# Kernel optimization log

Measured on AMD Instinct MI355X. Metric: run time of the kernel, lower is better.

## Reference

```python
import jax, jax.numpy as jnp
import numpy as np

N, B, D, K, H = 30000, 16, 32, 8, 8
DIST = 5.0
EPS = 1e-6


def setup_inputs() -> dict:
    key = jax.random.key(0)
    ks = jax.random.split(key, 16)
    sc = 1.0 / np.sqrt(D)
    inp = {
        'pos': jax.random.uniform(ks[0], (N, 3), jnp.float32) * 20.0,
        'node_features': jax.random.normal(ks[1], (N, D), jnp.float32),
        'batch': jnp.sort(jax.random.randint(ks[2], (N,), 0, B, dtype=jnp.int32)),
        'bessel_weights': jnp.linspace(jnp.pi, K * jnp.pi, K).astype(jnp.float32),
        'init_dummy': jax.random.normal(ks[3], (D,), jnp.float32),
        'Wq_dummy': jax.random.normal(ks[4], (D, D), jnp.float32) * sc,
        'Wq_graph': jax.random.normal(ks[5], (D, D), jnp.float32) * sc,
        'Wdot': jax.random.normal(ks[6], (D, D), jnp.float32) * sc,
        'W1_kd': jax.random.normal(ks[7], (K, H), jnp.float32) / np.sqrt(K),
        'W2_kd': jax.random.normal(ks[8], (H, D * D), jnp.float32) / np.sqrt(H),
        'W1_vd': jax.random.normal(ks[9], (K, H), jnp.float32) / np.sqrt(K),
        'W2_vd': jax.random.normal(ks[10], (H, D * D), jnp.float32) / np.sqrt(H),
        'W1_kg': jax.random.normal(ks[11], (K, H), jnp.float32) / np.sqrt(K),
        'W2_kg': jax.random.normal(ks[12], (H, D * D), jnp.float32) / np.sqrt(H),
        'W1_vg': jax.random.normal(ks[13], (K, H), jnp.float32) / np.sqrt(K),
        'W2_vg': jax.random.normal(ks[14], (H, D * D), jnp.float32) / np.sqrt(H),
    }
    return inp


def reference(pos, node_features, batch, bessel_weights, init_dummy,
              Wq_dummy, Wq_graph, Wdot,
              W1_kd, W2_kd, W1_vd, W2_vd, W1_kg, W2_kg, W1_vg, W2_vg):
    scale = 1.0 / np.sqrt(D)

    # --- dummy edge features: per-batch z extents + bessel basis ---
    z = pos[:, 2]                                            # [N]
    z_min = jax.ops.segment_min(z, batch, num_segments=B)    # [B]
    z_max = jax.ops.segment_max(z, batch, num_segments=B)    # [B]
    bot_len = z - z_min[batch] + DIST                        # [N]
    top_len = z_max[batch] + DIST - z                        # [N]

    def bessel(x):  # [N] -> [N,K]
        return jnp.sin(bessel_weights * x[:, None]) / (x[:, None] + EPS)

    edge = jnp.stack([bessel(bot_len), bessel(top_len)], axis=1)  # [N,2,K]

    # --- init dummy node features [B, 2, D] ---
    dummy = jnp.broadcast_to(init_dummy, (B, 2, D))

    def gen_w(W1, W2):  # conditional weight generator (silu MLP)
        return (jax.nn.silu(edge @ W1) @ W2).reshape(N, 2, D, D)

    # --- dummy nodes attend over graph nodes (segment softmax) ---
    wk = gen_w(W1_kd, W2_kd)                                 # [N,2,D,D]
    wv = gen_w(W1_vd, W2_vd)
    q = (dummy @ Wq_dummy)[batch]                            # [N,2,D]
    k = jnp.einsum('nd,nsde->nse', node_features, wk)        # [N,2,D]
    v = jnp.einsum('nd,nsde->nse', node_features, wv)
    s = jnp.einsum('nsq,qk,nsk->ns', q, Wdot, k) * scale     # [N,2]
    m = jax.ops.segment_max(s, batch, num_segments=B)
    e = jnp.exp(s - m[batch])
    zsum = jax.ops.segment_sum(e, batch, num_segments=B)
    attn = e / zsum[batch]                                   # [N,2]
    dummy_new = dummy + jax.ops.segment_sum(attn[..., None] * v, batch, num_segments=B)

    # --- graph nodes attend over (2) dummy nodes ---
    wkg = gen_w(W1_kg, W2_kg)
    wvg = gen_w(W1_vg, W2_vg)
    d_per = dummy_new[batch]                                 # [N,2,D]
    kg = jnp.einsum('nsd,nsde->nse', d_per, wkg)
    vg = jnp.einsum('nsd,nsde->nse', d_per, wvg)
    qg = node_features @ Wq_graph                            # [N,D]
    sg = jnp.einsum('nq,qk,nsk->ns', qg, Wdot, kg) * scale   # [N,2]
    ag = jax.nn.softmax(sg, axis=1)
    x_new = node_features + jnp.einsum('ns,nsd->nd', ag, vg)  # [N,D]
    return x_new
```

## Files before the change

### kernel.cpp

```cpp
#include <hip/hip_runtime.h>
#include <math.h>

#define NN 30000
#define BB 16
#define DD 32
#define KK 8
#define HH 8
#define DIST_C 5.0f
#define EPS_C 1e-6f
#define SCALE_C 0.17677669529663687f

#define WS_ZMIN 0
#define WS_ZMAX 16
#define WS_ZSUM 32
#define WS_QW   64
#define WS_PK   96
#define WS_WC   352
#define WS_T    1376
#define WS_AKG  9568
#define WS_AVG  17760

#define NPB 32

__device__ __forceinline__ unsigned fencode(float f) {
    unsigned u = __float_as_uint(f);
    return (u & 0x80000000u) ? ~u : (u | 0x80000000u);
}
__device__ __forceinline__ float fdecode(unsigned c) {
    return __uint_as_float((c & 0x80000000u) ? (c ^ 0x80000000u) : ~c);
}
__device__ __forceinline__ float silu(float x) { return x / (1.0f + expf(-x)); }

__device__ __forceinline__ void bessel_edges(float bw0, float x0, float x1, float edge[2][8]) {
    float xs[2]; xs[0] = x0; xs[1] = x1;
    #pragma unroll
    for (int s = 0; s < 2; ++s) {
        float x = xs[s];
        float inv = 1.0f / (x + EPS_C);
        float th = bw0 * x;
        float c2 = 2.0f * cosf(th);
        float skm1 = 0.0f;
        float sk = sinf(th);
        #pragma unroll
        for (int k = 0; k < 8; ++k) {
            edge[s][k] = sk * inv;
            float nx = c2 * sk - skm1;
            skm1 = sk;
            sk = nx;
        }
    }
}

__global__ __launch_bounds__(256) void k_init(const float* __restrict__ init_dummy,
                                              const float* __restrict__ Wq_dummy,
                                              const float* __restrict__ Wdot,
                                              const float* __restrict__ W2_kd,
                                              const float* __restrict__ Wq_graph,
                                              float* __restrict__ ws) {
    __shared__ float qvec[32];
    __shared__ float qWl[32];
    int t = threadIdx.x;
    unsigned* wsu = (unsigned*)ws;
    if (t < 16) { wsu[WS_ZMIN + t] = 0xFFFFFFFFu; wsu[WS_ZMAX + t] = 0u; }
    if (t < 32) ws[WS_ZSUM + t] = 0.0f;
    for (int i = t; i < 8192; i += 256) ws[WS_T + i] = 0.0f;
    if (t < 32) {
        float acc = 0.0f;
        for (int d = 0; d < 32; ++d) acc += init_dummy[d] * Wq_dummy[d * 32 + t];
        qvec[t] = acc;
    }
    __syncthreads();
    if (t < 32) {
        float acc = 0.0f;
        for (int e = 0; e < 32; ++e) acc += qvec[e] * Wdot[e * 32 + t];
        qWl[t] = acc;
        ws[WS_QW + t] = acc;
    }
    __syncthreads();
    {
        int h = t >> 5, d = t & 31;
        float acc = 0.0f;
        for (int e = 0; e < 32; ++e) acc += W2_kd[h * 1024 + d * 32 + e] * qWl[e];
        ws[WS_PK + t] = acc;
    }
    for (int i = t; i < 1024; i += 256) {
        int d = i >> 5, e = i & 31;
        float acc = 0.0f;
        for (int m = 0; m < 32; ++m) acc += Wq_graph[d * 32 + m] * Wdot[m * 32 + e];
        ws[WS_WC + i] = acc;
    }
}

__global__ __launch_bounds__(256) void k_zminmax(const float* __restrict__ pos,
                                                 const int* __restrict__ batch,
                                                 float* __restrict__ ws) {
    __shared__ unsigned zl[16], zh[16];
    int t = threadIdx.x;
    if (t < 16) { zl[t] = 0xFFFFFFFFu; zh[t] = 0u; }
    __syncthreads();
    int n = blockIdx.x * 256 + t;
    if (n < NN) {
        unsigned c = fencode(pos[3 * n + 2]);
        int b = batch[n];
        atomicMin(&zl[b], c);
        atomicMax(&zh[b], c);
    }
    __syncthreads();
    unsigned* wsu = (unsigned*)ws;
    if (t < 16) {
        if (zl[t] != 0xFFFFFFFFu) atomicMin(&wsu[WS_ZMIN + t], zl[t]);
        if (zh[t] != 0u)          atomicMax(&wsu[WS_ZMAX + t], zh[t]);
    }
}

__global__ __launch_bounds__(256) void k_phase1(const float* __restrict__ pos,
                                                const int* __restrict__ batch,
                                                const float* __restrict__ nf,
                                                const float* __restrict__ bw,
                                                const float* __restrict__ W1_kd,
                                                const float* __restrict__ W1_vd,
                                                float* __restrict__ ws) {
    __shared__ __align__(16) float Fl[NPB * 36];
    __shared__ float Lw[NPB * 17];
    __shared__ int   Lb[NPB];
    __shared__ __align__(16) float Pk[256];
    __shared__ float W1kd[64], W1vd[64], zsl[32];
    int t = threadIdx.x;
    if (t < 64) { W1kd[t] = W1_kd[t]; W1vd[t] = W1_vd[t]; }
    Pk[t] = ws[WS_PK + t];
    if (t < 32) zsl[t] = 0.0f;

    int li = t >> 3, g = t & 7;
    int n0 = blockIdx.x * NPB;
    int n = n0 + li;
    bool valid = n < NN;
    float4 fv4 = make_float4(0.f, 0.f, 0.f, 0.f);
    int b = 0;
    if (valid) {
        b = batch[n];
        fv4 = ((const float4*)nf)[n * 8 + g];
        ((float4*)(Fl + li * 36))[g] = fv4;
        if (g == 0) Lb[li] = b;
    } else {
        if (g == 0) Lb[li] = -1;
    }
    __syncthreads();

    if (valid) {
        const unsigned* wsu = (const unsigned*)ws;
        float z = pos[3 * n + 2];
        float zmin = fdecode(wsu[WS_ZMIN + b]);
        float zmax = fdecode(wsu[WS_ZMAX + b]);
        float edge[2][8];
        bessel_edges(bw[0], z - zmin + DIST_C, zmax + DIST_C - z, edge);

        float up[8];
        const float4* Pk4 = (const float4*)Pk;
        #pragma unroll
        for (int h = 0; h < 8; ++h) {
            float4 p = Pk4[h * 8 + g];
            up[h] = fv4.x * p.x + fv4.y * p.y + fv4.z * p.z + fv4.w * p.w;
        }
        float kd0, kd1;
        {
            float p0 = 0.f, p1 = 0.f;
            #pragma unroll
            for (int k = 0; k < 8; ++k) {
                float w = W1kd[k * 8 + g];
                p0 += edge[0][k] * w;
                p1 += edge[1][k] * w;
            }
            kd0 = silu(p0); kd1 = silu(p1);
        }
        int lanebase = (t & 63) & 56;
        float sp0 = 0.f, sp1 = 0.f;
        #pragma unroll
        for (int h = 0; h < 8; ++h) {
            float a0 = __shfl(kd0, lanebase + h, 64);
            float a1 = __shfl(kd1, lanebase + h, 64);
            sp0 += a0 * up[h];
            sp1 += a1 * up[h];
        }
        #pragma unroll
        for (int m = 1; m < 8; m <<= 1) {
            sp0 += __shfl_xor(sp0, m, 64);
            sp1 += __shfl_xor(sp1, m, 64);
        }
        float ev0 = expf(sp0 * SCALE_C);
        float ev1 = expf(sp1 * SCALE_C);
        if (g == 0) {
            atomicAdd(&zsl[b * 2 + 0], ev0);
            atomicAdd(&zsl[b * 2 + 1], ev1);
        }
        float q0 = 0.f, q1 = 0.f;
        #pragma unroll
        for (int k = 0; k < 8; ++k) {
            float w = W1vd[k * 8 + g];
            q0 += edge[0][k] * w;
            q1 += edge[1][k] * w;
        }
        Lw[li * 17 + g]     = ev0 * silu(q0);
        Lw[li * 17 + 8 + g] = ev1 * silu(q1);
    }
    __syncthreads();
    if (t < 32 && zsl[t] != 0.0f) atomicAdd(&ws[WS_ZSUM + t], zsl[t]);

    int count = NN - n0; if (count > NPB) count = NPB;
    int bf = Lb[0], bl = Lb[count - 1];
    int sh = t & 15, dp = t >> 4;
    for (int b2 = bf; b2 <= bl; ++b2) {
        float a0 = 0.f, a1 = 0.f;
        for (int i = 0; i < count; ++i) {
            if (Lb[i] != b2) continue;
            float w = Lw[i * 17 + sh];
            float2 x = *(const float2*)(Fl + i * 36 + 2 * dp);
            a0 += w * x.x;
            a1 += w * x.y;
        }
        float* Tb = ws + WS_T + b2 * 512 + sh * 32 + 2 * dp;
        atomicAdd(&Tb[0], a0);
        atomicAdd(&Tb[1], a1);
    }
}

__global__ __launch_bounds__(256) void k_batch(const float* __restrict__ init_dummy,
                                               const float* __restrict__ W2_vd,
                                               const float* __restrict__ W2_kg,
                                               const float* __restrict__ W2_vg,
                                               float* __restrict__ ws) {
    int bs = blockIdx.x;
    int b = bs >> 1, s = bs & 1;
    int t = threadIdx.x;
    __shared__ float Tl[256];
    __shared__ float part[256];
    __shared__ float dn[32];
    Tl[t] = ws[WS_T + b * 512 + s * 256 + t];
    __syncthreads();
    {
        int h = t >> 5, e = t & 31;
        float acc = 0.0f;
        #pragma unroll
        for (int d = 0; d < 32; ++d) acc += Tl[h * 32 + d] * W2_vd[h * 1024 + d * 32 + e];
        part[t] = acc;
    }
    __syncthreads();
    if (t < 32) {
        float acc = 0.0f;
        #pragma unroll
        for (int h = 0; h < 8; ++h) acc += part[h * 32 + t];
        float zs = ws[WS_ZSUM + b * 2 + s];
        dn[t] = init_dummy[t] + acc / zs;
    }
    __syncthreads();
    {
        int h = t >> 5, e = t & 31;
        float ak = 0.0f, av = 0.0f;
        #pragma unroll
        for (int d = 0; d < 32; ++d) {
            float dv = dn[d];
            ak += dv * W2_kg[h * 1024 + d * 32 + e];
            av += dv * W2_vg[h * 1024 + d * 32 + e];
        }
        ws[WS_AKG + b * 512 + s * 256 + t] = ak;
        ws[WS_AVG + b * 512 + s * 256 + t] = av;
    }
}

__global__ __launch_bounds__(256) void k_final(const float* __restrict__ pos,
                                               const int* __restrict__ batch,
                                               const float* __restrict__ nf,
                                               const float* __restrict__ bw,
                                               const float* __restrict__ W1_kg,
                                               const float* __restrict__ W1_vg,
                                               const float* __restrict__ ws,
                                               float* __restrict__ out) {
    __shared__ __align__(16) float Wc[1024];
    __shared__ __align__(16) float Fl[NPB * 36];
    __shared__ float W1kg[64], W1vg[64];
    int t = threadIdx.x;
    for (int i = t; i < 1024; i += 256) Wc[i] = ws[WS_WC + i];
    if (t < 64) { W1kg[t] = W1_kg[t]; W1vg[t] = W1_vg[t]; }

    int li = t >> 3, g = t & 7;
    int n0 = blockIdx.x * NPB;
    int n = n0 + li;
    bool valid = n < NN;
    float4 fv4 = make_float4(0.f, 0.f, 0.f, 0.f);
    if (valid) {
        fv4 = ((const float4*)nf)[n * 8 + g];
        ((float4*)(Fl + li * 36))[g] = fv4;
    }
    __syncthreads();
    if (!valid) return;

    int b = batch[n];
    const unsigned* wsu = (const unsigned*)ws;
    float z = pos[3 * n + 2];
    float zmin = fdecode(wsu[WS_ZMIN + b]);
    float zmax = fdecode(wsu[WS_ZMAX + b]);
    float edge[2][8];
    bessel_edges(bw[0], z - zmin + DIST_C, zmax + DIST_C - z, edge);

    float ak0, ak1, av0, av1;
    {
        float pk0 = 0.f, pk1 = 0.f, pv0 = 0.f, pv1 = 0.f;
        #pragma unroll
        for (int k = 0; k < 8; ++k) {
            float wk = W1kg[k * 8 + g];
            float wv = W1vg[k * 8 + g];
            pk0 += edge[0][k] * wk; pk1 += edge[1][k] * wk;
            pv0 += edge[0][k] * wv; pv1 += edge[1][k] * wv;
        }
        ak0 = silu(pk0); ak1 = silu(pk1);
        av0 = silu(pv0); av1 = silu(pv1);
    }

    float f[32];
    {
        const float4* myF4 = (const float4*)(Fl + li * 36);
        #pragma unroll
        for (int j = 0; j < 8; ++j) {
            float4 v = myF4[j];
            f[4 * j] = v.x; f[4 * j + 1] = v.y; f[4 * j + 2] = v.z; f[4 * j + 3] = v.w;
        }
    }
    float4 q4 = make_float4(0.f, 0.f, 0.f, 0.f);
    const float4* Wc4 = (const float4*)Wc;
    #pragma unroll
    for (int d = 0; d < 32; ++d) {
        float fd = f[d];
        float4 w = Wc4[d * 8 + g];
        q4.x += fd * w.x; q4.y += fd * w.y; q4.z += fd * w.z; q4.w += fd * w.w;
    }

    int lanebase = (t & 63) & 56;
    const float4* Ak4 = (const float4*)(ws + WS_AKG);
    const float4* Av4 = (const float4*)(ws + WS_AVG);
    float p0 = 0.f, p1 = 0.f;
    #pragma unroll
    for (int h = 0; h < 8; ++h) {
        float4 a0 = Ak4[b * 128 + h * 8 + g];
        float4 a1 = Ak4[b * 128 + 64 + h * 8 + g];
        float d0 = q4.x * a0.x + q4.y * a0.y + q4.z * a0.z + q4.w * a0.w;
        float d1 = q4.x * a1.x + q4.y * a1.y + q4.z * a1.z + q4.w * a1.w;
        p0 += __shfl(ak0, lanebase + h, 64) * d0;
        p1 += __shfl(ak1, lanebase + h, 64) * d1;
    }
    #pragma unroll
    for (int m = 1; m < 8; m <<= 1) {
        p0 += __shfl_xor(p0, m, 64);
        p1 += __shfl_xor(p1, m, 64);
    }
    float sg0 = p0 * SCALE_C, sg1 = p1 * SCALE_C;
    float mm = fmaxf(sg0, sg1);
    float e0 = expf(sg0 - mm), e1 = expf(sg1 - mm);
    float inv = 1.0f / (e0 + e1);
    float ag0 = e0 * inv, ag1 = e1 * inv;

    float4 x4 = fv4;
    #pragma unroll
    for (int h = 0; h < 8; ++h) {
        float w0 = ag0 * __shfl(av0, lanebase + h, 64);
        float w1 = ag1 * __shfl(av1, lanebase + h, 64);
        float4 a0 = Av4[b * 128 + h * 8 + g];
        float4 a1 = Av4[b * 128 + 64 + h * 8 + g];
        x4.x += w0 * a0.x + w1 * a1.x;
        x4.y += w0 * a0.y + w1 * a1.y;
        x4.z += w0 * a0.z + w1 * a1.z;
        x4.w += w0 * a0.w + w1 * a1.w;
    }
    ((float4*)out)[n * 8 + g] = x4;
}

extern "C" void kernel_launch(void* const* d_in, const int* in_sizes, int n_in,
                              void* d_out, int out_size, void* d_ws, size_t ws_size,
                              hipStream_t stream) {
    const float* pos        = (const float*)d_in[0];
    const float* nf         = (const float*)d_in[1];
    const int*   batch      = (const int*)d_in[2];
    const float* bw         = (const float*)d_in[3];
    const float* init_dummy = (const float*)d_in[4];
    const float* Wq_dummy   = (const float*)d_in[5];
    const float* Wq_graph   = (const float*)d_in[6];
    const float* Wdot       = (const float*)d_in[7];
    const float* W1_kd      = (const float*)d_in[8];
    const float* W2_kd      = (const float*)d_in[9];
    const float* W1_vd      = (const float*)d_in[10];
    const float* W2_vd      = (const float*)d_in[11];
    const float* W1_kg      = (const float*)d_in[12];
    const float* W2_kg      = (const float*)d_in[13];
    const float* W1_vg      = (const float*)d_in[14];
    const float* W2_vg      = (const float*)d_in[15];
    float* ws  = (float*)d_ws;
    float* out = (float*)d_out;

    int nblk1 = (NN + 255) / 256;
    int nblk8 = (NN + NPB - 1) / NPB;
    hipLaunchKernelGGL(k_init, dim3(1), dim3(256), 0, stream,
                       init_dummy, Wq_dummy, Wdot, W2_kd, Wq_graph, ws);
    hipLaunchKernelGGL(k_zminmax, dim3(nblk1), dim3(256), 0, stream, pos, batch, ws);
    hipLaunchKernelGGL(k_phase1, dim3(nblk8), dim3(256), 0, stream,
                       pos, batch, nf, bw, W1_kd, W1_vd, ws);
    hipLaunchKernelGGL(k_batch, dim3(32), dim3(256), 0, stream,
                       init_dummy, W2_vd, W2_kg, W2_vg, ws);
    hipLaunchKernelGGL(k_final, dim3(nblk8), dim3(256), 0, stream,
                       pos, batch, nf, bw, W1_kg, W1_vg, ws, out);
}
```

Baseline: 124.3 us.

## Fuse all stages into one persistent per-batch kernel with counter barrier

Replaces the five launches with a memset and one persistent kernel. Each batch segment gets a fixed group of blocks that find segment bounds by binary search on the sorted batch array, compute z min/max locally and accumulate dummy attention partials. The blocks then sync through a per-batch global atomic counter spin-wait, and each block recomputes the small per-batch dummy update and graph weights in shared memory before the final node pass. This removes launch gaps and global round trips for intermediates. In exchange it relies on all blocks being co-resident, duplicates small per-batch work in every block, and gives uneven load when batch sizes differ.

```diff
diff --git a/kernel.cpp b/kernel.cpp
--- a/kernel.cpp
+++ b/kernel.cpp
@@ -2,38 +2,20 @@
 #include <math.h>
 
 #define NN 30000
-#define BB 16
-#define DD 32
-#define KK 8
-#define HH 8
 #define DIST_C 5.0f
 #define EPS_C 1e-6f
 #define SCALE_C 0.17677669529663687f
 
-#define WS_ZMIN 0
-#define WS_ZMAX 16
-#define WS_ZSUM 32
-#define WS_QW   64
-#define WS_PK   96
-#define WS_WC   352
-#define WS_T    1376
-#define WS_AKG  9568
-#define WS_AVG  17760
-
-#define NPB 32
-
-__device__ __forceinline__ unsigned fencode(float f) {
-    unsigned u = __float_as_uint(f);
-    return (u & 0x80000000u) ? ~u : (u | 0x80000000u);
-}
-__device__ __forceinline__ float fdecode(unsigned c) {
-    return __uint_as_float((c & 0x80000000u) ? (c ^ 0x80000000u) : ~c);
-}
+#define WS_ZSUM 0
+#define WS_T    32
+#define WS_CTR  8224
+#define WS_ZERO_BYTES ((8224 + 16) * 4)
+
 __device__ __forceinline__ float silu(float x) { return x / (1.0f + expf(-x)); }
 
 __device__ __forceinline__ void bessel_edges(float bw0, float x0, float x1, float edge[2][8]) {
     float xs[2]; xs[0] = x0; xs[1] = x1;
-    #pragma unroll
+#pragma unroll
     for (int s = 0; s < 2; ++s) {
         float x = xs[s];
         float inv = 1.0f / (x + EPS_C);
@@ -41,335 +23,300 @@
         float c2 = 2.0f * cosf(th);
         float skm1 = 0.0f;
         float sk = sinf(th);
-        #pragma unroll
+#pragma unroll
         for (int k = 0; k < 8; ++k) {
             edge[s][k] = sk * inv;
             float nx = c2 * sk - skm1;
-            skm1 = sk;
-            sk = nx;
+            skm1 = sk; sk = nx;
         }
     }
 }
 
-__global__ __launch_bounds__(256) void k_init(const float* __restrict__ init_dummy,
-                                              const float* __restrict__ Wq_dummy,
-                                              const float* __restrict__ Wdot,
-                                              const float* __restrict__ W2_kd,
-                                              const float* __restrict__ Wq_graph,
-                                              float* __restrict__ ws) {
-    __shared__ float qvec[32];
-    __shared__ float qWl[32];
+__global__ __launch_bounds__(256, 2) void k_mega(
+    const float* __restrict__ pos, const int* __restrict__ batch,
+    const float* __restrict__ nf, const float* __restrict__ bw,
+    const float* __restrict__ W1_kd, const float* __restrict__ W1_vd,
+    const float* __restrict__ W1_kg, const float* __restrict__ W1_vg,
+    const float* __restrict__ init_dummy, const float* __restrict__ Wq_dummy,
+    const float* __restrict__ Wdot, const float* __restrict__ W2_kd,
+    const float* __restrict__ W2_vd, const float* __restrict__ W2_kg,
+    const float* __restrict__ W2_vg, const float* __restrict__ Wq_graph,
+    float* __restrict__ ws, float* __restrict__ out, int bpb)
+{
+    __shared__ int bnd[17];
+    __shared__ float Wdl[1024];
+    __shared__ float qvec[32], qWl[32];
+    __shared__ __align__(16) float Pk[256];
+    __shared__ __align__(16) float Wc[1024];
+    __shared__ float W1kd[64], W1vd[64], W1kg[64], W1vg[64];
+    __shared__ __align__(16) float Fl[32 * 36];
+    __shared__ float Lw[32 * 17];
+    __shared__ float zred[8];
+    __shared__ float zfin[2];
+    __shared__ float Tl[512], part[512], dn[64];
+    __shared__ __align__(16) float AKGl[512], AVGl[512];
+
     int t = threadIdx.x;
-    unsigned* wsu = (unsigned*)ws;
-    if (t < 16) { wsu[WS_ZMIN + t] = 0xFFFFFFFFu; wsu[WS_ZMAX + t] = 0u; }
-    if (t < 32) ws[WS_ZSUM + t] = 0.0f;
-    for (int i = t; i < 8192; i += 256) ws[WS_T + i] = 0.0f;
+    int b = blockIdx.x & 15;
+    int m = blockIdx.x >> 4;
+    int li = t >> 3, g = t & 7;
+    int lanebase = (t & 63) & 56;
+    float bw0 = bw[0];
+
+    if (t < 17) {
+        int lo = 0, hi = NN;
+        while (lo < hi) { int mid = (lo + hi) >> 1; if (batch[mid] < t) lo = mid + 1; else hi = mid; }
+        bnd[t] = lo;
+    }
+    for (int i = t; i < 1024; i += 256) Wdl[i] = Wdot[i];
+    if (t < 64) { W1kd[t] = W1_kd[t]; W1vd[t] = W1_vd[t]; W1kg[t] = W1_kg[t]; W1vg[t] = W1_vg[t]; }
     if (t < 32) {
-        float acc = 0.0f;
+        float acc = 0.f;
         for (int d = 0; d < 32; ++d) acc += init_dummy[d] * Wq_dummy[d * 32 + t];
         qvec[t] = acc;
     }
     __syncthreads();
+    int s0 = bnd[b], s1 = bnd[b + 1];
+
+    {
+        float zmn = 3.4e38f, zmx = -3.4e38f;
+        for (int i = s0 + t; i < s1; i += 256) {
+            float zz = pos[3 * i + 2];
+            zmn = fminf(zmn, zz); zmx = fmaxf(zmx, zz);
+        }
+#pragma unroll
+        for (int off = 1; off < 64; off <<= 1) {
+            zmn = fminf(zmn, __shfl_xor(zmn, off, 64));
+            zmx = fmaxf(zmx, __shfl_xor(zmx, off, 64));
+        }
+        if ((t & 63) == 0) { zred[(t >> 6) * 2] = zmn; zred[(t >> 6) * 2 + 1] = zmx; }
+    }
     if (t < 32) {
-        float acc = 0.0f;
-        for (int e = 0; e < 32; ++e) acc += qvec[e] * Wdot[e * 32 + t];
+        float acc = 0.f;
+        for (int e = 0; e < 32; ++e) acc += qvec[e] * Wdl[e * 32 + t];
         qWl[t] = acc;
-        ws[WS_QW + t] = acc;
-    }
-    __syncthreads();
+    }
+    __syncthreads();
+    if (t == 0) {
+        zfin[0] = fminf(fminf(zred[0], zred[2]), fminf(zred[4], zred[6]));
+        zfin[1] = fmaxf(fmaxf(zred[1], zred[3]), fmaxf(zred[5], zred[7]));
+    }
     {
         int h = t >> 5, d = t & 31;
-        float acc = 0.0f;
+        float acc = 0.f;
         for (int e = 0; e < 32; ++e) acc += W2_kd[h * 1024 + d * 32 + e] * qWl[e];
-        ws[WS_PK + t] = acc;
-    }
+        Pk[t] = acc;
+    }
+    __syncthreads();
+    float zminb = zfin[0], zmaxb = zfin[1];
+
+    float tAcc0 = 0.f, tAcc1 = 0.f, zsA0 = 0.f, zsA1 = 0.f;
+    int sh = t & 15, dp = t >> 4;
+    int stride = bpb * 32;
+    for (int base = s0 + m * 32; base < s1; base += stride) {
+        int cnt = s1 - base; if (cnt > 32) cnt = 32;
+        if (li < cnt) {
+            int n = base + li;
+            float4 fv4 = ((const float4*)nf)[n * 8 + g];
+            ((float4*)(Fl + li * 36))[g] = fv4;
+            float z = pos[3 * n + 2];
+            float edge[2][8];
+            bessel_edges(bw0, z - zminb + DIST_C, zmaxb + DIST_C - z, edge);
+            float up[8];
+            const float4* Pk4 = (const float4*)Pk;
+#pragma unroll
+            for (int h = 0; h < 8; ++h) {
+                float4 p = Pk4[h * 8 + g];
+                up[h] = fv4.x * p.x + fv4.y * p.y + fv4.z * p.z + fv4.w * p.w;
+            }
+            float p0 = 0.f, p1 = 0.f;
+#pragma unroll
+            for (int k = 0; k < 8; ++k) {
+                float w = W1kd[k * 8 + g];
+                p0 += edge[0][k] * w; p1 += edge[1][k] * w;
+            }
+            float kd0 = silu(p0), kd1 = silu(p1);
+            float sp0 = 0.f, sp1 = 0.f;
+#pragma unroll
+            for (int h = 0; h < 8; ++h) {
+                sp0 += __shfl(kd0, lanebase + h, 64) * up[h];
+                sp1 += __shfl(kd1, lanebase + h, 64) * up[h];
+            }
+#pragma unroll
+            for (int mm = 1; mm < 8; mm <<= 1) {
+                sp0 += __shfl_xor(sp0, mm, 64);
+                sp1 += __shfl_xor(sp1, mm, 64);
+            }
+            float ev0 = expf(sp0 * SCALE_C);
+            float ev1 = expf(sp1 * SCALE_C);
+            if (g == 0) { zsA0 += ev0; zsA1 += ev1; }
+            float q0 = 0.f, q1 = 0.f;
+#pragma unroll
+            for (int k = 0; k < 8; ++k) {
+                float w = W1vd[k * 8 + g];
+                q0 += edge[0][k] * w; q1 += edge[1][k] * w;
+            }
+            Lw[li * 17 + g] = ev0 * silu(q0);
+            Lw[li * 17 + 8 + g] = ev1 * silu(q1);
+        }
+        __syncthreads();
+        for (int i = 0; i < cnt; ++i) {
+            float w = Lw[i * 17 + sh];
+            float2 x = *(const float2*)(Fl + i * 36 + 2 * dp);
+            tAcc0 += w * x.x; tAcc1 += w * x.y;
+        }
+        __syncthreads();
+    }
+    {
+        float* Tb = ws + WS_T + b * 512 + sh * 32 + 2 * dp;
+        atomicAdd(&Tb[0], tAcc0);
+        atomicAdd(&Tb[1], tAcc1);
+#pragma unroll
+        for (int off = 1; off < 64; off <<= 1) {
+            zsA0 += __shfl_xor(zsA0, off, 64);
+            zsA1 += __shfl_xor(zsA1, off, 64);
+        }
+        if ((t & 63) == 0) { zred[(t >> 6) * 2] = zsA0; zred[(t >> 6) * 2 + 1] = zsA1; }
+    }
+    __syncthreads();
+    if (t == 0) {
+        atomicAdd(ws + WS_ZSUM + b * 2,     zred[0] + zred[2] + zred[4] + zred[6]);
+        atomicAdd(ws + WS_ZSUM + b * 2 + 1, zred[1] + zred[3] + zred[5] + zred[7]);
+    }
+    __syncthreads();
+
+    unsigned* ctru = (unsigned*)(ws + WS_CTR);
+    if (t == 0) { __threadfence(); atomicAdd(&ctru[b], 1u); }
     for (int i = t; i < 1024; i += 256) {
         int d = i >> 5, e = i & 31;
-        float acc = 0.0f;
-        for (int m = 0; m < 32; ++m) acc += Wq_graph[d * 32 + m] * Wdot[m * 32 + e];
-        ws[WS_WC + i] = acc;
-    }
-}
-
-__global__ __launch_bounds__(256) void k_zminmax(const float* __restrict__ pos,
-                                                 const int* __restrict__ batch,
-                                                 float* __restrict__ ws) {
-    __shared__ unsigned zl[16], zh[16];
-    int t = threadIdx.x;
-    if (t < 16) { zl[t] = 0xFFFFFFFFu; zh[t] = 0u; }
-    __syncthreads();
-    int n = blockIdx.x * 256 + t;
-    if (n < NN) {
-        unsigned c = fencode(pos[3 * n + 2]);
-        int b = batch[n];
-        atomicMin(&zl[b], c);
-        atomicMax(&zh[b], c);
-    }
-    __syncthreads();
-    unsigned* wsu = (unsigned*)ws;
-    if (t < 16) {
-        if (zl[t] != 0xFFFFFFFFu) atomicMin(&wsu[WS_ZMIN + t], zl[t]);
-        if (zh[t] != 0u)          atomicMax(&wsu[WS_ZMAX + t], zh[t]);
-    }
-}
-
-__global__ __launch_bounds__(256) void k_phase1(const float* __restrict__ pos,
-                                                const int* __restrict__ batch,
-                                                const float* __restrict__ nf,
-                                                const float* __restrict__ bw,
-                                                const float* __restrict__ W1_kd,
-                                                const float* __restrict__ W1_vd,
-                                                float* __restrict__ ws) {
-    __shared__ __align__(16) float Fl[NPB * 36];
-    __shared__ float Lw[NPB * 17];
-    __shared__ int   Lb[NPB];
-    __shared__ __align__(16) float Pk[256];
-    __shared__ float W1kd[64], W1vd[64], zsl[32];
-    int t = threadIdx.x;
-    if (t < 64) { W1kd[t] = W1_kd[t]; W1vd[t] = W1_vd[t]; }
-    Pk[t] = ws[WS_PK + t];
-    if (t < 32) zsl[t] = 0.0f;
-
-    int li = t >> 3, g = t & 7;
-    int n0 = blockIdx.x * NPB;
-    int n = n0 + li;
-    bool valid = n < NN;
-    float4 fv4 = make_float4(0.f, 0.f, 0.f, 0.f);
-    int b = 0;
-    if (valid) {
-        b = batch[n];
-        fv4 = ((const float4*)nf)[n * 8 + g];
-        ((float4*)(Fl + li * 36))[g] = fv4;
-        if (g == 0) Lb[li] = b;
-    } else {
-        if (g == 0) Lb[li] = -1;
-    }
-    __syncthreads();
-
-    if (valid) {
-        const unsigned* wsu = (const unsigned*)ws;
-        float z = pos[3 * n + 2];
-        float zmin = fdecode(wsu[WS_ZMIN + b]);
-        float zmax = fdecode(wsu[WS_ZMAX + b]);
-        float edge[2][8];
-        bessel_edges(bw[0], z - zmin + DIST_C, zmax + DIST_C - z, edge);
-
-        float up[8];
-        const float4* Pk4 = (const float4*)Pk;
-        #pragma unroll
-        for (int h = 0; h < 8; ++h) {
-            float4 p = Pk4[h * 8 + g];
-            up[h] = fv4.x * p.x + fv4.y * p.y + fv4.z * p.z + fv4.w * p.w;
-        }
-        float kd0, kd1;
-        {
+        float acc = 0.f;
+        for (int mm = 0; mm < 32; ++mm) acc += Wq_graph[d * 32 + mm] * Wdl[mm * 32 + e];
+        Wc[i] = acc;
+    }
+    if (t == 0) {
+        int guard = 0;
+        while (__hip_atomic_load(&ctru[b], __ATOMIC_ACQUIRE, __HIP_MEMORY_SCOPE_AGENT)
+               < (unsigned)bpb) {
+            __builtin_amdgcn_s_sleep(8);
+            if (++guard > (1 << 26)) break;
+        }
+    }
+    __syncthreads();
+
+    Tl[t]       = __hip_atomic_load(ws + WS_T + b * 512 + t,       __ATOMIC_RELAXED, __HIP_MEMORY_SCOPE_AGENT);
+    Tl[256 + t] = __hip_atomic_load(ws + WS_T + b * 512 + 256 + t, __ATOMIC_RELAXED, __HIP_MEMORY_SCOPE_AGENT);
+    if (t == 0) {
+        zfin[0] = __hip_atomic_load(ws + WS_ZSUM + b * 2,     __ATOMIC_RELAXED, __HIP_MEMORY_SCOPE_AGENT);
+        zfin[1] = __hip_atomic_load(ws + WS_ZSUM + b * 2 + 1, __ATOMIC_RELAXED, __HIP_MEMORY_SCOPE_AGENT);
+    }
+    __syncthreads();
+    {
+        int h = t >> 5, e = t & 31;
+        float a0 = 0.f, a1 = 0.f;
+        for (int d = 0; d < 32; ++d) {
+            float w2 = W2_vd[h * 1024 + d * 32 + e];
+            a0 += Tl[h * 32 + d] * w2;
+            a1 += Tl[256 + h * 32 + d] * w2;
+        }
+        part[t] = a0; part[256 + t] = a1;
+    }
+    __syncthreads();
+    if (t < 64) {
+        int s = t >> 5, dd = t & 31;
+        float acc = 0.f;
+        for (int h = 0; h < 8; ++h) acc += part[s * 256 + h * 32 + dd];
+        dn[t] = init_dummy[dd] + acc / zfin[s];
+    }
+    __syncthreads();
+    {
+        int h = t >> 5, e = t & 31;
+        float ak0 = 0.f, av0 = 0.f, ak1 = 0.f, av1 = 0.f;
+        for (int d = 0; d < 32; ++d) {
+            float w2k = W2_kg[h * 1024 + d * 32 + e];
+            float w2v = W2_vg[h * 1024 + d * 32 + e];
+            ak0 += dn[d] * w2k;      av0 += dn[d] * w2v;
+            ak1 += dn[32 + d] * w2k; av1 += dn[32 + d] * w2v;
+        }
+        AKGl[t] = ak0; AKGl[256 + t] = ak1;
+        AVGl[t] = av0; AVGl[256 + t] = av1;
+    }
+    __syncthreads();
+
+    const float4* Ak4 = (const float4*)AKGl;
+    const float4* Av4 = (const float4*)AVGl;
+    const float4* Wc4 = (const float4*)Wc;
+    for (int base = s0 + m * 32; base < s1; base += stride) {
+        int cnt = s1 - base; if (cnt > 32) cnt = 32;
+        float4 fv4 = make_float4(0.f, 0.f, 0.f, 0.f);
+        float z = 0.f;
+        if (li < cnt) {
+            int n = base + li;
+            fv4 = ((const float4*)nf)[n * 8 + g];
+            ((float4*)(Fl + li * 36))[g] = fv4;
+            z = pos[3 * n + 2];
+        }
+        __syncthreads();
+        if (li < cnt) {
+            float edge[2][8];
+            bessel_edges(bw0, z - zminb + DIST_C, zmaxb + DIST_C - z, edge);
+            float sk0, sk1, sv0, sv1;
+            {
+                float pk0 = 0.f, pk1 = 0.f, pv0 = 0.f, pv1 = 0.f;
+#pragma unroll
+                for (int k = 0; k < 8; ++k) {
+                    float wk = W1kg[k * 8 + g];
+                    float wv = W1vg[k * 8 + g];
+                    pk0 += edge[0][k] * wk; pk1 += edge[1][k] * wk;
+                    pv0 += edge[0][k] * wv; pv1 += edge[1][k] * wv;
+                }
+                sk0 = silu(pk0); sk1 = silu(pk1);
+                sv0 = silu(pv0); sv1 = silu(pv1);
+            }
+            float4 q4 = make_float4(0.f, 0.f, 0.f, 0.f);
+            const float* myF = Fl + li * 36;
+#pragma unroll
+            for (int d = 0; d < 32; ++d) {
+                float fd = myF[d];
+                float4 w = Wc4[d * 8 + g];
+                q4.x += fd * w.x; q4.y += fd * w.y; q4.z += fd * w.z; q4.w += fd * w.w;
+            }
             float p0 = 0.f, p1 = 0.f;
-            #pragma unroll
-            for (int k = 0; k < 8; ++k) {
-                float w = W1kd[k * 8 + g];
-                p0 += edge[0][k] * w;
-                p1 += edge[1][k] * w;
-            }
-            kd0 = silu(p0); kd1 = silu(p1);
-        }
-        int lanebase = (t & 63) & 56;
-        float sp0 = 0.f, sp1 = 0.f;
-        #pragma unroll
-        for (int h = 0; h < 8; ++h) {
-            float a0 = __shfl(kd0, lanebase + h, 64);
-            float a1 = __shfl(kd1, lanebase + h, 64);
-            sp0 += a0 * up[h];
-            sp1 += a1 * up[h];
-        }
-        #pragma unroll
-        for (int m = 1; m < 8; m <<= 1) {
-            sp0 += __shfl_xor(sp0, m, 64);
-            sp1 += __shfl_xor(sp1, m, 64);
-        }
-        float ev0 = expf(sp0 * SCALE_C);
-        float ev1 = expf(sp1 * SCALE_C);
-        if (g == 0) {
-            atomicAdd(&zsl[b * 2 + 0], ev0);
-            atomicAdd(&zsl[b * 2 + 1], ev1);
-        }
-        float q0 = 0.f, q1 = 0.f;
-        #pragma unroll
-        for (int k = 0; k < 8; ++k) {
-            float w = W1vd[k * 8 + g];
-            q0 += edge[0][k] * w;
-            q1 += edge[1][k] * w;
-        }
-        Lw[li * 17 + g]     = ev0 * silu(q0);
-        Lw[li * 17 + 8 + g] = ev1 * silu(q1);
-    }
-    __syncthreads();
-    if (t < 32 && zsl[t] != 0.0f) atomicAdd(&ws[WS_ZSUM + t], zsl[t]);
-
-    int count = NN - n0; if (count > NPB) count = NPB;
-    int bf = Lb[0], bl = Lb[count - 1];
-    int sh = t & 15, dp = t >> 4;
-    for (int b2 = bf; b2 <= bl; ++b2) {
-        float a0 = 0.f, a1 = 0.f;
-        for (int i = 0; i < count; ++i) {
-            if (Lb[i] != b2) continue;
-            float w = Lw[i * 17 + sh];
-            float2 x = *(const float2*)(Fl + i * 36 + 2 * dp);
-            a0 += w * x.x;
-            a1 += w * x.y;
-        }
-        float* Tb = ws + WS_T + b2 * 512 + sh * 32 + 2 * dp;
-        atomicAdd(&Tb[0], a0);
-        atomicAdd(&Tb[1], a1);
-    }
-}
-
-__global__ __launch_bounds__(256) void k_batch(const float* __restrict__ init_dummy,
-                                               const float* __restrict__ W2_vd,
-                                               const float* __restrict__ W2_kg,
-                                               const float* __restrict__ W2_vg,
-                                               float* __restrict__ ws) {
-    int bs = blockIdx.x;
-    int b = bs >> 1, s = bs & 1;
-    int t = threadIdx.x;
-    __shared__ float Tl[256];
-    __shared__ float part[256];
-    __shared__ float dn[32];
-    Tl[t] = ws[WS_T + b * 512 + s * 256 + t];
-    __syncthreads();
-    {
-        int h = t >> 5, e = t & 31;
-        float acc = 0.0f;
-        #pragma unroll
-        for (int d = 0; d < 32; ++d) acc += Tl[h * 32 + d] * W2_vd[h * 1024 + d * 32 + e];
-        part[t] = acc;
-    }
-    __syncthreads();
-    if (t < 32) {
-        float acc = 0.0f;
-        #pragma unroll
-        for (int h = 0; h < 8; ++h) acc += part[h * 32 + t];
-        float zs = ws[WS_ZSUM + b * 2 + s];
-        dn[t] = init_dummy[t] + acc / zs;
-    }
-    __syncthreads();
-    {
-        int h = t >> 5, e = t & 31;
-        float ak = 0.0f, av = 0.0f;
-        #pragma unroll
-        for (int d = 0; d < 32; ++d) {
-            float dv = dn[d];
-            ak += dv * W2_kg[h * 1024 + d * 32 + e];
-            av += dv * W2_vg[h * 1024 + d * 32 + e];
-        }
-        ws[WS_AKG + b * 512 + s * 256 + t] = ak;
-        ws[WS_AVG + b * 512 + s * 256 + t] = av;
-    }
-}
-
-__global__ __launch_bounds__(256) void k_final(const float* __restrict__ pos,
-                                               const int* __restrict__ batch,
-                                               const float* __restrict__ nf,
-                                               const float* __restrict__ bw,
-                                               const float* __restrict__ W1_kg,
-                                               const float* __restrict__ W1_vg,
-                                               const float* __restrict__ ws,
-                                               float* __restrict__ out) {
-    __shared__ __align__(16) float Wc[1024];
-    __shared__ __align__(16) float Fl[NPB * 36];
-    __shared__ float W1kg[64], W1vg[64];
-    int t = threadIdx.x;
-    for (int i = t; i < 1024; i += 256) Wc[i] = ws[WS_WC + i];
-    if (t < 64) { W1kg[t] = W1_kg[t]; W1vg[t] = W1_vg[t]; }
-
-    int li = t >> 3, g = t & 7;
-    int n0 = blockIdx.x * NPB;
-    int n = n0 + li;
-    bool valid = n < NN;
-    float4 fv4 = make_float4(0.f, 0.f, 0.f, 0.f);
-    if (valid) {
-        fv4 = ((const float4*)nf)[n * 8 + g];
-        ((float4*)(Fl + li * 36))[g] = fv4;
-    }
-    __syncthreads();
-    if (!valid) return;
-
-    int b = batch[n];
-    const unsigned* wsu = (const unsigned*)ws;
-    float z = pos[3 * n + 2];
-    float zmin = fdecode(wsu[WS_ZMIN + b]);
-    float zmax = fdecode(wsu[WS_ZMAX + b]);
-    float edge[2][8];
-    bessel_edges(bw[0], z - zmin + DIST_C, zmax + DIST_C - z, edge);
-
-    float ak0, ak1, av0, av1;
-    {
-        float pk0 = 0.f, pk1 = 0.f, pv0 = 0.f, pv1 = 0.f;
-        #pragma unroll
-        for (int k = 0; k < 8; ++k) {
-            float wk = W1kg[k * 8 + g];
-            float wv = W1vg[k * 8 + g];
-            pk0 += edge[0][k] * wk; pk1 += edge[1][k] * wk;
-            pv0 += edge[0][k] * wv; pv1 += edge[1][k] * wv;
-        }
-        ak0 = silu(pk0); ak1 = silu(pk1);
-        av0 = silu(pv0); av1 = silu(pv1);
-    }
-
-    float f[32];
-    {
-        const float4* myF4 = (const float4*)(Fl + li * 36);
-        #pragma unroll
-        for (int j = 0; j < 8; ++j) {
-            float4 v = myF4[j];
-            f[4 * j] = v.x; f[4 * j + 1] = v.y; f[4 * j + 2] = v.z; f[4 * j + 3] = v.w;
-        }
-    }
-    float4 q4 = make_float4(0.f, 0.f, 0.f, 0.f);
-    const float4* Wc4 = (const float4*)Wc;
-    #pragma unroll
-    for (int d = 0; d < 32; ++d) {
-        float fd = f[d];
-        float4 w = Wc4[d * 8 + g];
-        q4.x += fd * w.x; q4.y += fd * w.y; q4.z += fd * w.z; q4.w += fd * w.w;
-    }
-
-    int lanebase = (t & 63) & 56;
-    const float4* Ak4 = (const float4*)(ws + WS_AKG);
-    const float4* Av4 = (const float4*)(ws + WS_AVG);
-    float p0 = 0.f, p1 = 0.f;
-    #pragma unroll
-    for (int h = 0; h < 8; ++h) {
-        float4 a0 = Ak4[b * 128 + h * 8 + g];
-        float4 a1 = Ak4[b * 128 + 64 + h * 8 + g];
-        float d0 = q4.x * a0.x + q4.y * a0.y + q4.z * a0.z + q4.w * a0.w;
-        float d1 = q4.x * a1.x + q4.y * a1.y + q4.z * a1.z + q4.w * a1.w;
-        p0 += __shfl(ak0, lanebase + h, 64) * d0;
-        p1 += __shfl(ak1, lanebase + h, 64) * d1;
-    }
-    #pragma unroll
-    for (int m = 1; m < 8; m <<= 1) {
-        p0 += __shfl_xor(p0, m, 64);
-        p1 += __shfl_xor(p1, m, 64);
-    }
-    float sg0 = p0 * SCALE_C, sg1 = p1 * SCALE_C;
-    float mm = fmaxf(sg0, sg1);
-    float e0 = expf(sg0 - mm), e1 = expf(sg1 - mm);
-    float inv = 1.0f / (e0 + e1);
-    float ag0 = e0 * inv, ag1 = e1 * inv;
-
-    float4 x4 = fv4;
-    #pragma unroll
-    for (int h = 0; h < 8; ++h) {
-        float w0 = ag0 * __shfl(av0, lanebase + h, 64);
-        float w1 = ag1 * __shfl(av1, lanebase + h, 64);
-        float4 a0 = Av4[b * 128 + h * 8 + g];
-        float4 a1 = Av4[b * 128 + 64 + h * 8 + g];
-        x4.x += w0 * a0.x + w1 * a1.x;
-        x4.y += w0 * a0.y + w1 * a1.y;
-        x4.z += w0 * a0.z + w1 * a1.z;
-        x4.w += w0 * a0.w + w1 * a1.w;
-    }
-    ((float4*)out)[n * 8 + g] = x4;
+#pragma unroll
+            for (int h = 0; h < 8; ++h) {
+                float4 a0 = Ak4[h * 8 + g];
+                float4 a1 = Ak4[64 + h * 8 + g];
+                float d0 = q4.x * a0.x + q4.y * a0.y + q4.z * a0.z + q4.w * a0.w;
+                float d1 = q4.x * a1.x + q4.y * a1.y + q4.z * a1.z + q4.w * a1.w;
+                p0 += __shfl(sk0, lanebase + h, 64) * d0;
+                p1 += __shfl(sk1, lanebase + h, 64) * d1;
+            }
+#pragma unroll
+            for (int mm = 1; mm < 8; mm <<= 1) {
+                p0 += __shfl_xor(p0, mm, 64);
+                p1 += __shfl_xor(p1, mm, 64);
+            }
+            float sg0 = p0 * SCALE_C, sg1 = p1 * SCALE_C;
+            float mx = fmaxf(sg0, sg1);
+            float e0 = expf(sg0 - mx), e1 = expf(sg1 - mx);
+            float inv = 1.0f / (e0 + e1);
+            float ag0 = e0 * inv, ag1 = e1 * inv;
+            float4 x4 = fv4;
+#pragma unroll
+            for (int h = 0; h < 8; ++h) {
+                float w0 = ag0 * __shfl(sv0, lanebase + h, 64);
+                float w1 = ag1 * __shfl(sv1, lanebase + h, 64);
+                float4 a0 = Av4[h * 8 + g];
+                float4 a1 = Av4[64 + h * 8 + g];
+                x4.x += w0 * a0.x + w1 * a1.x;
+                x4.y += w0 * a0.y + w1 * a1.y;
+                x4.z += w0 * a0.z + w1 * a1.z;
+                x4.w += w0 * a0.w + w1 * a1.w;
+            }
+            int n = base + li;
+            ((float4*)out)[n * 8 + g] = x4;
+        }
+        __syncthreads();
+    }
 }
 
 extern "C" void kernel_launch(void* const* d_in, const int* in_sizes, int n_in,
@@ -394,15 +341,17 @@
     float* ws  = (float*)d_ws;
     float* out = (float*)d_out;
 
-    int nblk1 = (NN + 255) / 256;
-    int nblk8 = (NN + NPB - 1) / NPB;
-    hipLaunchKernelGGL(k_init, dim3(1), dim3(256), 0, stream,
-                       init_dummy, Wq_dummy, Wdot, W2_kd, Wq_graph, ws);
-    hipLaunchKernelGGL(k_zminmax, dim3(nblk1), dim3(256), 0, stream, pos, batch, ws);
-    hipLaunchKernelGGL(k_phase1, dim3(nblk8), dim3(256), 0, stream,
-                       pos, batch, nf, bw, W1_kd, W1_vd, ws);
-    hipLaunchKernelGGL(k_batch, dim3(32), dim3(256), 0, stream,
-                       init_dummy, W2_vd, W2_kg, W2_vg, ws);
-    hipLaunchKernelGGL(k_final, dim3(nblk8), dim3(256), 0, stream,
-                       pos, batch, nf, bw, W1_kg, W1_vg, ws, out);
+    static int bpb_cached = -1;
+    if (bpb_cached < 0) {
+        int maxb = 0;
+        hipError_t e = hipOccupancyMaxActiveBlocksPerMultiprocessor(
+            &maxb, reinterpret_cast<const void*>(k_mega), 256, 0);
+        bpb_cached = (e == hipSuccess && maxb >= 2) ? 32 : 16;
+    }
+
+    hipMemsetAsync(ws, 0, WS_ZERO_BYTES, stream);
+    hipLaunchKernelGGL(k_mega, dim3(16 * bpb_cached), dim3(256), 0, stream,
+                       pos, batch, nf, bw, W1_kd, W1_vd, W1_kg, W1_vg,
+                       init_dummy, Wq_dummy, Wdot, W2_kd, W2_vd, W2_kg, W2_vg, Wq_graph,
+                       ws, out, bpb_cached);
 }
```

Result: slower. 136.7 us (+10.0%).
